# Kernel optimization log

Measured on AMD Instinct MI355X. Metric: run time of the kernel, lower is better.

The kernel has to match this reference:

```python
import jax, jax.numpy as jnp
import numpy as np

KMIX = 16
N_CH = 302   # hardcoded number of output channels in MDNLayer
N_POS = 394  # hardcoded evaluation grid size


def setup_inputs() -> dict:
    key = jax.random.key(0)
    k1, k2 = jax.random.split(key)
    B, D = 32, 1024
    units = N_CH * KMIX * 3  # 14496
    x = jax.random.normal(k1, (B, D), dtype=jnp.float32)
    # 'random_normal' keras initializer uses stddev=0.05
    w = jax.random.normal(k2, (D, units), dtype=jnp.float32) * 0.05
    b = jnp.zeros((units,), dtype=jnp.float32)
    return {"x": x, "w": w, "b": b}


def reference(x, w, b):
    B = x.shape[0]
    # Dense projection then reshape to (B, 3*KMIX, 302) as in the original
    y = (x @ w + b).reshape(B, 3 * KMIX, N_CH)
    mu = y[:, 0 * KMIX:1 * KMIX, :]   # (B, K, 302)
    sig = y[:, 1 * KMIX:2 * KMIX, :]  # (B, K, 302) used raw as Normal scale
    pi = y[:, 2 * KMIX:3 * KMIX, :]   # (B, K, 302) mixture logits

    pos = jnp.linspace(0.0, 1.0, N_POS, dtype=x.dtype)  # (394,)
    inv_sqrt_2pi = jnp.asarray(1.0 / np.sqrt(2.0 * np.pi), dtype=x.dtype)

    # Per-component Normal pdf at each grid point: (B, K, 302, 394)
    z = (pos[None, None, None, :] - mu[..., None]) / sig[..., None]
    comp_pdf = jnp.exp(-0.5 * z * z) * (inv_sqrt_2pi / sig[..., None])

    # Mixture weights: softmax over the K components (axis=1)
    weights = jax.nn.softmax(pi, axis=1)  # (B, K, 302)

    # Weighted sum over components -> (B, 302, 394)
    res = jnp.einsum('bkc,bkcp->bcp', weights, comp_pdf)
    return res[..., None]  # (B, 302, 394, 1)
```

## Files before the change

### kernel.cpp

```cpp
#include <hip/hip_runtime.h>

#define BATCH 32
#define DIM 1024
#define NCH 302
#define KMIX 16
#define UNITS 14496
#define NPOS 394
#define KSPLIT 16
#define KCHUNK (DIM / KSPLIT)
#define NTILE 256
#define NTILES 57
#define BSUB 8
#define NPAIRS (BATCH * NCH)

__global__ __launch_bounds__(256) void gemm_kernel(
    const float* __restrict__ x, const float* __restrict__ w,
    float* __restrict__ partial)
{
  __shared__ float xs[BATCH][KCHUNK];
  const int tid = threadIdx.x;
  const int kch = blockIdx.x / NTILES;
  const int tile = blockIdx.x - kch * NTILES;
  const int k0  = kch * KCHUNK;
  const int n0  = tile * NTILE;

#pragma unroll
  for (int j = 0; j < 2; ++j) {
    const int idx4 = tid + j * 256;
    const int b    = idx4 >> 4;
    const int d4   = idx4 & 15;
    *(float4*)(&xs[b][d4 * 4]) = *(const float4*)(x + b * DIM + k0 + d4 * 4);
  }
  __syncthreads();

  const int lane = tid & 63;
  const int bg   = tid >> 6;
  const bool st  = (n0 + lane * 4) < UNITS;
  int nc = n0 + lane * 4;
  if (nc > UNITS - 4) nc = UNITS - 4;

  float4 acc[BSUB];
#pragma unroll
  for (int bi = 0; bi < BSUB; ++bi) acc[bi] = make_float4(0.f, 0.f, 0.f, 0.f);

  const float* wp = w + (size_t)k0 * UNITS + nc;
  float4 wa[4], wb[4];
#pragma unroll
  for (int j = 0; j < 4; ++j) wa[j] = *(const float4*)(wp + (size_t)j * UNITS);
#pragma unroll
  for (int j = 0; j < 4; ++j) wb[j] = *(const float4*)(wp + (size_t)(4 + j) * UNITS);

  for (int dd = 0; dd < KCHUNK; dd += 8) {
    const int nx = dd + 8;
    float4 wa2[4], wb2[4];
    if (nx < KCHUNK) {
#pragma unroll
      for (int j = 0; j < 4; ++j)
        wa2[j] = *(const float4*)(wp + (size_t)(nx + j) * UNITS);
    }
#pragma unroll
    for (int bi = 0; bi < BSUB; ++bi) {
      const float4 xv = *(const float4*)(&xs[bg * BSUB + bi][dd]);
      acc[bi].x = fmaf(xv.x, wa[0].x, acc[bi].x);
      acc[bi].y = fmaf(xv.x, wa[0].y, acc[bi].y);
      acc[bi].z = fmaf(xv.x, wa[0].z, acc[bi].z);
      acc[bi].w = fmaf(xv.x, wa[0].w, acc[bi].w);
      acc[bi].x = fmaf(xv.y, wa[1].x, acc[bi].x);
      acc[bi].y = fmaf(xv.y, wa[1].y, acc[bi].y);
      acc[bi].z = fmaf(xv.y, wa[1].z, acc[bi].z);
      acc[bi].w = fmaf(xv.y, wa[1].w, acc[bi].w);
      acc[bi].x = fmaf(xv.z, wa[2].x, acc[bi].x);
      acc[bi].y = fmaf(xv.z, wa[2].y, acc[bi].y);
      acc[bi].z = fmaf(xv.z, wa[2].z, acc[bi].z);
      acc[bi].w = fmaf(xv.z, wa[2].w, acc[bi].w);
      acc[bi].x = fmaf(xv.w, wa[3].x, acc[bi].x);
      acc[bi].y = fmaf(xv.w, wa[3].y, acc[bi].y);
      acc[bi].z = fmaf(xv.w, wa[3].z, acc[bi].z);
      acc[bi].w = fmaf(xv.w, wa[3].w, acc[bi].w);
    }
    if (nx < KCHUNK) {
#pragma unroll
      for (int j = 0; j < 4; ++j)
        wb2[j] = *(const float4*)(wp + (size_t)(nx + 4 + j) * UNITS);
    }
#pragma unroll
    for (int bi = 0; bi < BSUB; ++bi) {
      const float4 xv = *(const float4*)(&xs[bg * BSUB + bi][dd + 4]);
      acc[bi].x = fmaf(xv.x, wb[0].x, acc[bi].x);
      acc[bi].y = fmaf(xv.x, wb[0].y, acc[bi].y);
      acc[bi].z = fmaf(xv.x, wb[0].z, acc[bi].z);
      acc[bi].w = fmaf(xv.x, wb[0].w, acc[bi].w);
      acc[bi].x = fmaf(xv.y, wb[1].x, acc[bi].x);
      acc[bi].y = fmaf(xv.y, wb[1].y, acc[bi].y);
      acc[bi].z = fmaf(xv.y, wb[1].z, acc[bi].z);
      acc[bi].w = fmaf(xv.y, wb[1].w, acc[bi].w);
      acc[bi].x = fmaf(xv.z, wb[2].x, acc[bi].x);
      acc[bi].y = fmaf(xv.z, wb[2].y, acc[bi].y);
      acc[bi].z = fmaf(xv.z, wb[2].z, acc[bi].z);
      acc[bi].w = fmaf(xv.z, wb[2].w, acc[bi].w);
      acc[bi].x = fmaf(xv.w, wb[3].x, acc[bi].x);
      acc[bi].y = fmaf(xv.w, wb[3].y, acc[bi].y);
      acc[bi].z = fmaf(xv.w, wb[3].z, acc[bi].z);
      acc[bi].w = fmaf(xv.w, wb[3].w, acc[bi].w);
    }
    if (nx < KCHUNK) {
#pragma unroll
      for (int j = 0; j < 4; ++j) { wa[j] = wa2[j]; wb[j] = wb2[j]; }
    }
  }

  if (st) {
    float* pp = partial + ((size_t)kch * BATCH + bg * BSUB) * UNITS + nc;
#pragma unroll
    for (int bi = 0; bi < BSUB; ++bi)
      *(float4*)(pp + (size_t)bi * UNITS) = acc[bi];
  }
}

__global__ __launch_bounds__(256) void reduce_kernel(
    const float* __restrict__ partial, const float* __restrict__ bias,
    float* __restrict__ yt)
{
  const int idx  = blockIdx.x * 256 + threadIdx.x;
  const int base = idx * 4;
  float4 s4 = make_float4(0.f, 0.f, 0.f, 0.f);
#pragma unroll
  for (int k = 0; k < KSPLIT; ++k) {
    const float4 v = *(const float4*)(partial + (size_t)k * (BATCH * UNITS) + base);
    s4.x += v.x; s4.y += v.y; s4.z += v.z; s4.w += v.w;
  }
  const int b = base / UNITS;
  const int n = base - b * UNITS;
  const float4 bv = *(const float4*)(bias + n);
  s4.x += bv.x; s4.y += bv.y; s4.z += bv.z; s4.w += bv.w;

  float vs[4] = {s4.x, s4.y, s4.z, s4.w};
#pragma unroll
  for (int j = 0; j < 4; ++j) {
    const int nj = n + j;
    const int s  = nj / NCH;
    const int c  = nj - s * NCH;
    yt[((size_t)b * NCH + c) * 48 + s] = vs[j];
  }
}

__global__ __launch_bounds__(256) void mdn_kernel(
    const float* __restrict__ yt, float* __restrict__ out)
{
  __shared__ float ps[4][48];
  const int tid  = threadIdx.x;
  const int lane = tid & 63;
  const int bg   = tid >> 6;

  if (tid < 192) ps[tid / 48][tid % 48] = yt[(size_t)blockIdx.x * 192 + tid];
  __syncthreads();

  const int pair = blockIdx.x * 4 + bg;
  const float* pp = ps[bg];

  float pw[KMIX];
  float m = -3.4e38f;
#pragma unroll
  for (int k = 0; k < KMIX; ++k) {
    pw[k] = pp[32 + k];
    m = fmaxf(m, pw[k]);
  }
  float ssum = 0.0f;
#pragma unroll
  for (int k = 0; k < KMIX; ++k) { pw[k] = __expf(pw[k] - m); ssum += pw[k]; }
  const float wnorm = 0.39894228040143267f / ssum;

  float posv[7];
#pragma unroll
  for (int i = 0; i < 7; ++i)
    posv[i] = (float)(lane + i * 64) * (1.0f / (NPOS - 1));

  float acc[7] = {0.f, 0.f, 0.f, 0.f, 0.f, 0.f, 0.f};
#pragma unroll
  for (int k = 0; k < KMIX; ++k) {
    const float mu   = pp[k];
    const float sig  = pp[16 + k];
    const float isig = 1.0f / sig;
    const float coef = pw[k] * wnorm * isig;
    const float nmu  = -mu * isig;
#pragma unroll
    for (int i = 0; i < 7; ++i) {
      const float t = fmaf(posv[i], isig, nmu);
      acc[i] = fmaf(coef, exp2f(t * t * -0.72134752044448170f), acc[i]);
    }
  }

  float* op = out + (size_t)pair * NPOS;
#pragma unroll
  for (int i = 0; i < 7; ++i) {
    const int p = lane + i * 64;
    if (p < NPOS) op[p] = acc[i];
  }
}

extern "C" void kernel_launch(void* const* d_in, const int* in_sizes, int n_in,
                              void* d_out, int out_size, void* d_ws, size_t ws_size,
                              hipStream_t stream) {
  const float* x    = (const float*)d_in[0];
  const float* w    = (const float*)d_in[1];
  const float* bias = (const float*)d_in[2];
  float* out     = (float*)d_out;
  float* partial = (float*)d_ws;
  float* yt      = (float*)((char*)d_ws + (size_t)32 * 1024 * 1024);

  gemm_kernel<<<NTILES * KSPLIT, 256, 0, stream>>>(x, w, partial);
  reduce_kernel<<<(BATCH * UNITS / 4) / 256, 256, 0, stream>>>(partial, bias, yt);
  mdn_kernel<<<NPAIRS / 4, 256, 0, stream>>>(yt, out);
}
```

Before: 143.6 us.

## Fuse split-K reduction into MDN kernel and halve the K split

Removes the separate reduce kernel and the transposed intermediate buffer: the MDN kernel now sums the split-K partials plus bias directly while loading its per-pair parameters. KSPLIT drops from 16 to 8, which halves the partial-sum traffic and the number of reads per parameter, and the x staging loop is widened to fill the larger K chunk. The cost is fewer GEMM blocks (456 instead of 912), so there is less parallelism for streaming w. The fused loads are also strided gathers across the partial buffer, where the old reduce kernel read it coalesced.

After: 138.9 us. 1.03x faster.

```diff
diff --git a/kernel.cpp b/kernel.cpp
--- a/kernel.cpp
+++ b/kernel.cpp
@@ -6,7 +6,7 @@
 #define KMIX 16
 #define UNITS 14496
 #define NPOS 394
-#define KSPLIT 16
+#define KSPLIT 8
 #define KCHUNK (DIM / KSPLIT)
 #define NTILE 256
 #define NTILES 57
@@ -25,10 +25,10 @@
   const int n0  = tile * NTILE;
 
 #pragma unroll
-  for (int j = 0; j < 2; ++j) {
+  for (int j = 0; j < 4; ++j) {
     const int idx4 = tid + j * 256;
-    const int b    = idx4 >> 4;
-    const int d4   = idx4 & 15;
+    const int b    = idx4 >> 5;
+    const int d4   = idx4 & 31;
     *(float4*)(&xs[b][d4 * 4]) = *(const float4*)(x + b * DIM + k0 + d4 * 4);
   }
   __syncthreads();
@@ -117,45 +117,32 @@
   }
 }
 
-__global__ __launch_bounds__(256) void reduce_kernel(
+__global__ __launch_bounds__(256) void mdn_kernel(
     const float* __restrict__ partial, const float* __restrict__ bias,
-    float* __restrict__ yt)
-{
-  const int idx  = blockIdx.x * 256 + threadIdx.x;
-  const int base = idx * 4;
-  float4 s4 = make_float4(0.f, 0.f, 0.f, 0.f);
-#pragma unroll
-  for (int k = 0; k < KSPLIT; ++k) {
-    const float4 v = *(const float4*)(partial + (size_t)k * (BATCH * UNITS) + base);
-    s4.x += v.x; s4.y += v.y; s4.z += v.z; s4.w += v.w;
-  }
-  const int b = base / UNITS;
-  const int n = base - b * UNITS;
-  const float4 bv = *(const float4*)(bias + n);
-  s4.x += bv.x; s4.y += bv.y; s4.z += bv.z; s4.w += bv.w;
-
-  float vs[4] = {s4.x, s4.y, s4.z, s4.w};
-#pragma unroll
-  for (int j = 0; j < 4; ++j) {
-    const int nj = n + j;
-    const int s  = nj / NCH;
-    const int c  = nj - s * NCH;
-    yt[((size_t)b * NCH + c) * 48 + s] = vs[j];
-  }
-}
-
-__global__ __launch_bounds__(256) void mdn_kernel(
-    const float* __restrict__ yt, float* __restrict__ out)
+    float* __restrict__ out)
 {
   __shared__ float ps[4][48];
   const int tid  = threadIdx.x;
   const int lane = tid & 63;
   const int bg   = tid >> 6;
+  const int p0   = blockIdx.x * 4;
 
-  if (tid < 192) ps[tid / 48][tid % 48] = yt[(size_t)blockIdx.x * 192 + tid];
+  if (tid < 192) {
+    const int pi = tid / 48;
+    const int s  = tid - pi * 48;
+    const int pr = p0 + pi;
+    const int b  = pr / NCH;
+    const int c  = pr - b * NCH;
+    const int n  = s * NCH + c;
+    float sum = bias[n];
+#pragma unroll
+    for (int k = 0; k < KSPLIT; ++k)
+      sum += partial[((size_t)k * BATCH + b) * UNITS + n];
+    ps[pi][s] = sum;
+  }
   __syncthreads();
 
-  const int pair = blockIdx.x * 4 + bg;
+  const int pair = p0 + bg;
   const float* pp = ps[bg];
 
   float pw[KMIX];
@@ -206,9 +193,7 @@
   const float* bias = (const float*)d_in[2];
   float* out     = (float*)d_out;
   float* partial = (float*)d_ws;
-  float* yt      = (float*)((char*)d_ws + (size_t)32 * 1024 * 1024);
 
   gemm_kernel<<<NTILES * KSPLIT, 256, 0, stream>>>(x, w, partial);
-  reduce_kernel<<<(BATCH * UNITS / 4) / 256, 256, 0, stream>>>(partial, bias, yt);
-  mdn_kernel<<<NPAIRS / 4, 256, 0, stream>>>(yt, out);
+  mdn_kernel<<<NPAIRS / 4, 256, 0, stream>>>(partial, bias, out);
 }
```
